# Kernel optimization log

Measured on AMD Instinct MI355X. Metric: run time of the kernel, lower is better.

## Reference

```python
import jax, jax.numpy as jnp
import numpy as np

N_NODES = 100000
N_REL = 7
E = 1600000
D_IN = 128
D_H = 256
D_OUT = 2
EPS = 1e-5


def setup_inputs() -> dict:
    key = jax.random.key(0)
    ks = jax.random.split(key, 16)
    s = 0.05
    features = jax.random.normal(ks[0], (N_NODES, D_IN), jnp.float32)
    edges = jax.random.randint(ks[1], (N_REL, 2, E), 0, N_NODES)
    return {
        "features": features,
        "edges": edges,
        # layer 1 SAGE weights (per relation): fc_self, fc_neigh, bias
        "Wself1": jax.random.normal(ks[2], (N_REL, D_IN, D_H), jnp.float32) * s,
        "Wneigh1": jax.random.normal(ks[3], (N_REL, D_IN, D_H), jnp.float32) * s,
        "b1": jax.random.normal(ks[4], (N_REL, D_H), jnp.float32) * s,
        # layer 2
        "Wself2": jax.random.normal(ks[5], (N_REL, D_H, D_H), jnp.float32) * s,
        "Wneigh2": jax.random.normal(ks[6], (N_REL, D_H, D_H), jnp.float32) * s,
        "b2": jax.random.normal(ks[7], (N_REL, D_H), jnp.float32) * s,
        # LayerNorm params for 2 layers
        "ln_g": jnp.ones((2, D_H), jnp.float32),
        "ln_b": jnp.zeros((2, D_H), jnp.float32),
        # classifier: Linear -> ReLU -> BatchNorm1d(eval) -> Linear
        "Wc1": jax.random.normal(ks[8], (D_H, D_H // 2), jnp.float32) * s,
        "bc1": jnp.zeros((D_H // 2,), jnp.float32),
        "bn_g": jnp.ones((D_H // 2,), jnp.float32),
        "bn_b": jnp.zeros((D_H // 2,), jnp.float32),
        "Wc2": jax.random.normal(ks[9], (D_H // 2, D_OUT), jnp.float32) * s,
        "bc2": jnp.zeros((D_OUT,), jnp.float32),
    }


def _layer_norm(x, g, b):
    mu = jnp.mean(x, axis=-1, keepdims=True)
    var = jnp.var(x, axis=-1, keepdims=True)
    return (x - mu) * jax.lax.rsqrt(var + EPS) * g + b


def _hetero_sage(x, edges, Wself, Wneigh, b):
    # DGL SAGEConv('mean'): out = x @ W_self + mean_neigh(x) @ W_neigh + bias,
    # then HeteroGraphConv aggregate='mean' over relations.
    n = x.shape[0]
    acc = jnp.zeros((n, Wself.shape[-1]), x.dtype)
    for r in range(edges.shape[0]):  # fixed small relation set
        src, dst = edges[r, 0], edges[r, 1]
        msum = jax.ops.segment_sum(x[src], dst, num_segments=n)
        deg = jax.ops.segment_sum(jnp.ones((src.shape[0],), x.dtype), dst, num_segments=n)
        mean = msum / jnp.maximum(deg, 1.0)[:, None]
        acc = acc + x @ Wself[r] + mean @ Wneigh[r] + b[r]
    return acc / edges.shape[0]


def reference(features, edges, Wself1, Wneigh1, b1, Wself2, Wneigh2, b2,
              ln_g, ln_b, Wc1, bc1, bn_g, bn_b, Wc2, bc2):
    # layer 1: hetero conv -> LayerNorm -> ReLU (dropout = identity in eval)
    h = _hetero_sage(features, edges, Wself1, Wneigh1, b1)
    h = jax.nn.relu(_layer_norm(h, ln_g[0], ln_b[0]))
    # layer 2
    h = _hetero_sage(h, edges, Wself2, Wneigh2, b2)
    h = jax.nn.relu(_layer_norm(h, ln_g[1], ln_b[1]))
    # classifier: Linear -> ReLU -> BatchNorm1d(eval: running_mean=0, running_var=1) -> Linear
    z = jax.nn.relu(h @ Wc1 + bc1)
    z = z * (bn_g * jax.lax.rsqrt(jnp.float32(1.0 + EPS))) + bn_b
    return z @ Wc2 + bc2
```

## Files before the change

### kernel.cpp

```cpp
#include <hip/hip_runtime.h>
#include <hip/hip_bf16.h>
#include <cstdint>


#define NN 100000
#define NREL 7
#define NE 1600000
#define NB 128
#define BCAP 14336
#define BNODES 782

using uint = unsigned int;
using ushort_t = unsigned short;
using bf16x8 = __attribute__((ext_vector_type(8))) __bf16;
using f32x4 = __attribute__((ext_vector_type(4))) float;

__device__ __forceinline__ ushort_t f32_to_bf16(float f) {
    uint u = __float_as_uint(f);
    u += 0x7fffu + ((u >> 16) & 1u);
    return (ushort_t)(u >> 16);
}
__device__ __forceinline__ float bf16lo(uint u) { return __uint_as_float(u << 16); }
__device__ __forceinline__ float bf16hi(uint u) { return __uint_as_float(u & 0xffff0000u); }

__device__ __forceinline__ void gload16(const ushort_t* g, ushort_t* l) {
    __builtin_amdgcn_global_load_lds(
        (const __attribute__((address_space(1))) uint*)g,
        (__attribute__((address_space(3))) uint*)l, 16, 0, 0);
}

__global__ __launch_bounds__(256) void binpass_k(const int* __restrict__ edges,
                                                 int* __restrict__ bcnt,
                                                 int* __restrict__ bsrc,
                                                 int* __restrict__ bdst) {
    __shared__ int cnt[NB];
    __shared__ int lofs[NB];
    __shared__ int gbase[NB];
    __shared__ int wtot[2];
    __shared__ int stotal;
    __shared__ uint2 stage[4096];
    __shared__ unsigned char bb[4096];
    int r = blockIdx.y;
    int t = threadIdx.x;
    if (t < NB) cnt[t] = 0;
    __syncthreads();
    int e0 = blockIdx.x * 4096;
    uint2 mypair[16];
    int myrb[16];
#pragma unroll
    for (int i = 0; i < 16; ++i) {
        int e = e0 + i * 256 + t;
        if (e < NE) {
            int s = edges[(size_t)(2 * r) * NE + e];
            int d = edges[(size_t)(2 * r + 1) * NE + e];
            int b = d / BNODES;
            int rank = atomicAdd(&cnt[b], 1);
            myrb[i] = (rank << 7) | b;
            mypair[i] = make_uint2((uint)s, (uint)d);
        } else {
            myrb[i] = -1;
        }
    }
    __syncthreads();
    {
        int c = (t < NB) ? cnt[t] : 0;
        int lane = t & 63, wv = t >> 6;
        int x = c;
#pragma unroll
        for (int off = 1; off < 64; off <<= 1) {
            int y = __shfl_up(x, off);
            if (lane >= off) x += y;
        }
        if (t < NB && lane == 63) wtot[wv] = x;
        __syncthreads();
        if (t < NB) {
            int excl = x - c + (wv ? wtot[0] : 0);
            lofs[t] = excl;
            gbase[t] = atomicAdd(&bcnt[r * NB + t], c);
            if (t == NB - 1) stotal = excl + c;
        }
    }
    __syncthreads();
#pragma unroll
    for (int i = 0; i < 16; ++i) {
        if (myrb[i] >= 0) {
            int b = myrb[i] & 127;
            int p = lofs[b] + (myrb[i] >> 7);
            stage[p] = mypair[i];
            bb[p] = (unsigned char)b;
        }
    }
    __syncthreads();
    int total = stotal;
    for (int p = t; p < total; p += 256) {
        int b = bb[p];
        uint2 pr = stage[p];
        int gpos = gbase[b] + (p - lofs[b]);
        if (gpos < BCAP) {
            size_t o = ((size_t)r * NB + b) * BCAP + gpos;
            bsrc[o] = (int)pr.x;
            bdst[o] = (int)pr.y;
        }
    }
}

__global__ __launch_bounds__(1024) void deg_bucket_k(const int* __restrict__ bdst,
                                                     const int* __restrict__ bcnt,
                                                     int* __restrict__ deg) {
    __shared__ int hist[BNODES];
    int rb = blockIdx.x;
    int r = rb >> 7, b = rb & 127;
    int node0 = b * BNODES;
    int nnodes = NN - node0 < BNODES ? NN - node0 : BNODES;
    int t = threadIdx.x;
    for (int i = t; i < nnodes; i += 1024) hist[i] = 0;
    __syncthreads();
    int cb = bcnt[rb];
    if (cb > BCAP) cb = BCAP;
    const int* src = bdst + (size_t)rb * BCAP;
    for (int i = t; i < cb; i += 1024) {
        atomicAdd(&hist[src[i] - node0], 1);
    }
    __syncthreads();
    for (int i = t; i < nnodes; i += 1024) deg[r * NN + node0 + i] = hist[i];
}

__global__ void scan1_k(const int* __restrict__ deg, int* __restrict__ rowptr,
                        int* __restrict__ blk, int total) {
    __shared__ int wsum[4];
    int t = threadIdx.x;
    int base = blockIdx.x * 4096 + t * 16;
    int vals[16];
    int s = 0;
#pragma unroll
    for (int i = 0; i < 16; ++i) {
        int g = base + i;
        int v = (g < total) ? deg[g] : 0;
        vals[i] = s;
        s += v;
    }
    int lane = t & 63, w = t >> 6;
    int x = s;
    for (int off = 1; off < 64; off <<= 1) {
        int y = __shfl_up(x, off);
        if (lane >= off) x += y;
    }
    if (lane == 63) wsum[w] = x;
    __syncthreads();
    if (t == 0) {
        int a = 0;
#pragma unroll
        for (int k = 0; k < 4; ++k) { int b = wsum[k]; wsum[k] = a; a += b; }
        blk[blockIdx.x] = a;
    }
    __syncthreads();
    int excl = x - s + wsum[w];
#pragma unroll
    for (int i = 0; i < 16; ++i) {
        int g = base + i;
        if (g < total) rowptr[g] = excl + vals[i];
    }
}

__global__ void scan2_k(int* blk, int nb) {
    if (threadIdx.x == 0 && blockIdx.x == 0) {
        int a = 0;
        for (int i = 0; i < nb; ++i) { int b = blk[i]; blk[i] = a; a += b; }
    }
}

__global__ void scan3_k(int* __restrict__ rowptr, const int* __restrict__ blk, int total) {
    int t = threadIdx.x;
    int add = blk[blockIdx.x];
    int base = blockIdx.x * 4096 + t * 16;
#pragma unroll
    for (int i = 0; i < 16; ++i) {
        int g = base + i;
        if (g < total) rowptr[g] += add;
    }
}

__global__ __launch_bounds__(1024) void bucket_sort_k(const int* __restrict__ bsrc,
                                                      const int* __restrict__ bdst,
                                                      const int* __restrict__ bcnt,
                                                      const int* __restrict__ rowptr,
                                                      int* __restrict__ csr) {
    __shared__ int stage[BCAP];
    __shared__ int lcur[BNODES];
    int rb = blockIdx.x;
    int r = rb >> 7, b = rb & 127;
    int node0 = b * BNODES;
    int nnodes = NN - node0 < BNODES ? NN - node0 : BNODES;
    int t = threadIdx.x;
    int rowbase = rowptr[r * NN + node0];
    int endIdx = r * NN + node0 + nnodes;
    int rowend = (endIdx < NREL * NN) ? rowptr[endIdx] : (NREL * NE);
    int truen = rowend - rowbase;
    int nent = truen < BCAP ? truen : BCAP;
    for (int i = t; i < nent; i += 1024) stage[i] = 0;
    for (int i = t; i < nnodes; i += 1024) lcur[i] = 0;
    __syncthreads();
    int cb = bcnt[rb];
    if (cb > BCAP) cb = BCAP;
    for (int i = t; i < cb; i += 1024) {
        int node = bdst[(size_t)rb * BCAP + i];
        int sv = bsrc[(size_t)rb * BCAP + i];
        int pos = rowptr[r * NN + node] - rowbase + atomicAdd(&lcur[node - node0], 1);
        if (pos < BCAP) stage[pos] = sv;
    }
    __syncthreads();
    for (int i = t; i < nent; i += 1024) csr[rowbase + i] = stage[i];
    for (int i = nent + t; i < truen; i += 1024) csr[rowbase + i] = 0;
}

__global__ void convert_x_k(const float* __restrict__ x, ushort_t* __restrict__ xb) {
    int idx = blockIdx.x * 256 + threadIdx.x;
    int n = idx >> 5;
    int c = idx & 31;
    float4 v = *(const float4*)(x + (size_t)n * 128 + c * 4);
    ushort4 o;
    o.x = f32_to_bf16(v.x); o.y = f32_to_bf16(v.y);
    o.z = f32_to_bf16(v.z); o.w = f32_to_bf16(v.w);
    *(ushort4*)(xb + (size_t)n * 128 + c * 4) = o;
}

__global__ void prep_B1cat_k(const float* __restrict__ Wself, const float* __restrict__ Wneigh,
                             const float* __restrict__ b, ushort_t* __restrict__ Bcat,
                             float* __restrict__ bs) {
    int idx = blockIdx.x * 256 + threadIdx.x;
    if (idx < 262144) {
        int n = idx >> 10;
        int k = idx & 1023;
        float v;
        if (k < 128) {
            v = 0.f;
#pragma unroll
            for (int r = 0; r < 7; ++r) v += Wself[((size_t)r * 128 + k) * 256 + n];
        } else {
            int rel = (k >> 7) - 1;
            int k2 = k & 127;
            v = Wneigh[((size_t)rel * 128 + k2) * 256 + n];
        }
        Bcat[(size_t)n * 1024 + k] = f32_to_bf16(v);
    } else if (idx < 262400) {
        int i = idx - 262144;
        float s = 0.f;
#pragma unroll
        for (int r = 0; r < 7; ++r) s += b[r * 256 + i];
        bs[i] = s * (1.f / 7.f);
    }
}

__global__ void prep_B2cat_k(const float* __restrict__ Wself, const float* __restrict__ Wneigh,
                             const float* __restrict__ b, ushort_t* __restrict__ Bcat,
                             float* __restrict__ bs) {
    int idx = blockIdx.x * 256 + threadIdx.x;
    if (idx < 524288) {
        int n = idx >> 11;
        int k = idx & 2047;
        float v;
        if (k < 256) {
            v = 0.f;
#pragma unroll
            for (int r = 0; r < 7; ++r) v += Wself[((size_t)r * 256 + k) * 256 + n];
        } else {
            int rel = (k >> 8) - 1;
            int k2 = k & 255;
            v = Wneigh[((size_t)rel * 256 + k2) * 256 + n];
        }
        Bcat[(size_t)n * 2048 + k] = f32_to_bf16(v);
    } else if (idx < 524544) {
        int i = idx - 524288;
        float s = 0.f;
#pragma unroll
        for (int r = 0; r < 7; ++r) s += b[r * 256 + i];
        bs[i] = s * (1.f / 7.f);
    }
}

__global__ void prep_cls_k(const float* __restrict__ Wc1, const float* __restrict__ bn_g,
                           const float* __restrict__ bn_b, const float* __restrict__ Wc2,
                           const float* __restrict__ bc2, ushort_t* __restrict__ Wc1T,
                           float* __restrict__ W2p, float* __restrict__ cp) {
    int idx = blockIdx.x * 256 + threadIdx.x;
    if (idx < 128 * 256) {
        int n = idx >> 8;
        int k = idx & 255;
        Wc1T[(size_t)n * 256 + k] = f32_to_bf16(Wc1[(size_t)k * 128 + n]);
    } else if (idx < 128 * 256 + 256) {
        int e = idx - 128 * 256;
        int d = e >> 1, j = e & 1;
        W2p[e] = bn_g[d] * rsqrtf(1.f + 1e-5f) * Wc2[d * 2 + j];
    } else if (idx < 128 * 256 + 256 + 2) {
        int j = idx - (128 * 256 + 256);
        float s = bc2[j];
        for (int d = 0; d < 128; ++d) s += bn_b[d] * Wc2[d * 2 + j];
        cp[j] = s;
    }
}

template <int V>
__global__ __launch_bounds__(256) void gather_mean_k(
    const ushort_t* __restrict__ T, const int* __restrict__ csr,
    const int* __restrict__ rowptr, const int* __restrict__ deg,
    ushort_t* __restrict__ Mout, int r, int n0) {
    int n = n0 + blockIdx.x * 4 + (threadIdx.x >> 6);
    if (n >= NN) return;
    int lane = threadIdx.x & 63;
    int pair = r * NN + n;
    int start = rowptr[pair];
    int cnt = deg[pair];
    float aLo[2][2] = {{0.f, 0.f}, {0.f, 0.f}};
    float aHi[2][2] = {{0.f, 0.f}, {0.f, 0.f}};
    int j = 0;
    if (V == 1) {
        const uint* Tu = (const uint*)T;
        for (; j + 8 <= cnt; j += 8) {
            int s[8];
#pragma unroll
            for (int q = 0; q < 8; ++q) s[q] = csr[start + j + q];
            uint u[8];
#pragma unroll
            for (int q = 0; q < 8; ++q) u[q] = Tu[(size_t)s[q] * 64 + lane];
#pragma unroll
            for (int q = 0; q < 8; ++q) {
                aLo[0][q & 1] += bf16lo(u[q]);
                aHi[0][q & 1] += bf16hi(u[q]);
            }
        }
        for (; j < cnt; ++j) {
            uint u = Tu[(size_t)csr[start + j] * 64 + lane];
            aLo[0][0] += bf16lo(u);
            aHi[0][0] += bf16hi(u);
        }
        float inv = 1.f / (float)(cnt > 1 ? cnt : 1);
        uint lo = f32_to_bf16((aLo[0][0] + aLo[0][1]) * inv);
        uint hi = f32_to_bf16((aHi[0][0] + aHi[0][1]) * inv);
        ((uint*)(Mout + (size_t)(n - n0) * 128))[lane] = lo | (hi << 16);
    } else {
        const uint2* Tu = (const uint2*)T;
        for (; j + 8 <= cnt; j += 8) {
            int s[8];
#pragma unroll
            for (int q = 0; q < 8; ++q) s[q] = csr[start + j + q];
            uint2 u[8];
#pragma unroll
            for (int q = 0; q < 8; ++q) u[q] = Tu[(size_t)s[q] * 64 + lane];
#pragma unroll
            for (int q = 0; q < 8; ++q) {
                aLo[0][q & 1] += bf16lo(u[q].x);
                aHi[0][q & 1] += bf16hi(u[q].x);
                aLo[1][q & 1] += bf16lo(u[q].y);
                aHi[1][q & 1] += bf16hi(u[q].y);
            }
        }
        for (; j < cnt; ++j) {
            uint2 u = Tu[(size_t)csr[start + j] * 64 + lane];
            aLo[0][0] += bf16lo(u.x);
            aHi[0][0] += bf16hi(u.x);
            aLo[1][0] += bf16lo(u.y);
            aHi[1][0] += bf16hi(u.y);
        }
        float inv = 1.f / (float)(cnt > 1 ? cnt : 1);
        uint lox = f32_to_bf16((aLo[0][0] + aLo[0][1]) * inv);
        uint hix = f32_to_bf16((aHi[0][0] + aHi[0][1]) * inv);
        uint loy = f32_to_bf16((aLo[1][0] + aLo[1][1]) * inv);
        uint hiy = f32_to_bf16((aHi[1][0] + aHi[1][1]) * inv);
        ((uint2*)(Mout + (size_t)(n - n0) * 256))[lane] =
            make_uint2(lox | (hix << 16), loy | (hiy << 16));
    }
}

__global__ __launch_bounds__(256) void gemm_multi(
    const ushort_t* __restrict__ A0, const ushort_t* __restrict__ AM,
    int D, int lgD, int aoff, int Mseg, const ushort_t* __restrict__ BT,
    void* __restrict__ Cv, int M, int N, int K, float alpha,
    const float* __restrict__ bias, int mode) {
    __shared__ __align__(16) ushort_t lA[2 * 4096];
    __shared__ __align__(16) ushort_t lB[2 * 4096];
    int t = threadIdx.x;
    int gr0 = blockIdx.x * 128;
    int gc0 = blockIdx.y * 128;
    int w = t >> 6, lane = t & 63;
    int wr = w >> 1, wc = w & 1;
    int lm = lane & 15, quad = lane >> 4;
    int srow = lane >> 2;
    int schunk = (lane & 3) * 8;
    const ushort_t* A0s = A0 + (size_t)aoff * D;
    size_t segstride = (size_t)Mseg * D;
    f32x4 acc[4][4];
#pragma unroll
    for (int i = 0; i < 4; ++i)
#pragma unroll
        for (int j = 0; j < 4; ++j) acc[i][j] = (f32x4){0.f, 0.f, 0.f, 0.f};

    for (int kk = 0; kk < K; kk += 64) {
        int seg = kk >> lgD;
        int kloc = kk & (D - 1);
        const ushort_t* Asrc = (seg == 0) ? A0s : (AM + (size_t)(seg - 1) * segstride);
        __syncthreads();
#pragma unroll
        for (int s = 0; s < 2; ++s) {
#pragma unroll
            for (int j = 0; j < 2; ++j) {
                int rb = (j * 4 + w) * 16;
                int row = rb + srow;
                int gr = gr0 + row;
                if (gr < M)
                    gload16(Asrc + (size_t)gr * D + kloc + s * 32 + schunk,
                            lA + s * 4096 + rb * 32);
                gload16(BT + (size_t)(gc0 + row) * K + kk + s * 32 + schunk,
                        lB + s * 4096 + rb * 32);
            }
        }
        __syncthreads();
#pragma unroll
        for (int s = 0; s < 2; ++s) {
            bf16x8 af[4], bfr[4];
#pragma unroll
            for (int f = 0; f < 4; ++f) {
                af[f] = *(const bf16x8*)(lA + s * 4096 + (wr * 64 + f * 16 + lm) * 32 + quad * 8);
                bfr[f] = *(const bf16x8*)(lB + s * 4096 + (wc * 64 + f * 16 + lm) * 32 + quad * 8);
            }
#pragma unroll
            for (int fr = 0; fr < 4; ++fr)
#pragma unroll
                for (int fc = 0; fc < 4; ++fc)
                    acc[fr][fc] = __builtin_amdgcn_mfma_f32_16x16x32_bf16(
                        af[fr], bfr[fc], acc[fr][fc], 0, 0, 0);
        }
    }
    float* Cf = (float*)Cv;
    ushort_t* Cb = (ushort_t*)Cv;
#pragma unroll
    for (int fr = 0; fr < 4; ++fr) {
#pragma unroll
        for (int fc = 0; fc < 4; ++fc) {
#pragma unroll
            for (int i = 0; i < 4; ++i) {
                int row = wr * 64 + fr * 16 + quad * 4 + i;
                int col = wc * 64 + fc * 16 + lm;
                int gr = gr0 + row;
                int gc = gc0 + col;
                if (gr < M) {
                    size_t o = (size_t)gr * N + gc;
                    float v = acc[fr][fc][i] * alpha;
                    v += bias ? bias[gc] : 0.f;
                    if (mode == 4) {
                        Cf[o] = fmaxf(v, 0.f);
                    } else {
                        Cb[o] = f32_to_bf16(v);
                    }
                }
            }
        }
    }
}

__global__ __launch_bounds__(256) void ln_relu_b_k(
    const ushort_t* __restrict__ h, const float* __restrict__ g,
    const float* __restrict__ b, ushort_t* __restrict__ out) {
    int n = blockIdx.x * 4 + (threadIdx.x >> 6);
    if (n >= NN) return;
    int lane = threadIdx.x & 63;
    uint2 u = ((const uint2*)(h + (size_t)n * 256))[lane];
    float v0 = bf16lo(u.x), v1 = bf16hi(u.x), v2 = bf16lo(u.y), v3 = bf16hi(u.y);
    float s = v0 + v1 + v2 + v3;
    float q = v0 * v0 + v1 * v1 + v2 * v2 + v3 * v3;
#pragma unroll
    for (int m = 1; m < 64; m <<= 1) {
        s += __shfl_xor(s, m);
        q += __shfl_xor(q, m);
    }
    float mean = s * (1.f / 256.f);
    float var = q * (1.f / 256.f) - mean * mean;
    float rs = rsqrtf(var + 1e-5f);
    float4 gv = *(const float4*)(g + lane * 4);
    float4 bv = *(const float4*)(b + lane * 4);
    float y0 = fmaxf((v0 - mean) * rs * gv.x + bv.x, 0.f);
    float y1 = fmaxf((v1 - mean) * rs * gv.y + bv.y, 0.f);
    float y2 = fmaxf((v2 - mean) * rs * gv.z + bv.z, 0.f);
    float y3 = fmaxf((v3 - mean) * rs * gv.w + bv.w, 0.f);
    uint2 o;
    o.x = (uint)f32_to_bf16(y0) | ((uint)f32_to_bf16(y1) << 16);
    o.y = (uint)f32_to_bf16(y2) | ((uint)f32_to_bf16(y3) << 16);
    *(uint2*)(out + (size_t)n * 256 + lane * 4) = o;
}

__global__ __launch_bounds__(256) void final_k(const float* __restrict__ z1,
                                               const float* __restrict__ W2p,
                                               const float* __restrict__ cp,
                                               float* __restrict__ out) {
    int n = blockIdx.x * 4 + (threadIdx.x >> 6);
    if (n >= NN) return;
    int lane = threadIdx.x & 63;
    const float* zr = z1 + (size_t)n * 128;
    float z0 = zr[lane], z1v = zr[lane + 64];
    float a0 = z0 * W2p[lane * 2 + 0] + z1v * W2p[(lane + 64) * 2 + 0];
    float a1 = z0 * W2p[lane * 2 + 1] + z1v * W2p[(lane + 64) * 2 + 1];
#pragma unroll
    for (int m = 1; m < 64; m <<= 1) {
        a0 += __shfl_xor(a0, m);
        a1 += __shfl_xor(a1, m);
    }
    if (lane == 0) {
        out[(size_t)n * 2 + 0] = a0 + cp[0];
        out[(size_t)n * 2 + 1] = a1 + cp[1];
    }
}

constexpr size_t O_DEG   = 0;
constexpr size_t O_ROW   = 2800128;
constexpr size_t O_BLK   = 5600256;
constexpr size_t O_CSR   = 5601280;
constexpr size_t O_B1C   = 50401280;
constexpr size_t O_B2C   = 50925568;
constexpr size_t O_WC1T  = 51974144;
constexpr size_t O_W2P   = 52039680;
constexpr size_t O_CP    = 52040704;
constexpr size_t O_B1S   = 52040960;
constexpr size_t O_B2S   = 52041984;
constexpr size_t O_XB    = 52043008;
constexpr size_t O_MEAN1 = 77643008;
constexpr size_t O_HACC1 = 167243008;
constexpr size_t O_BCNT  = 52043008;
constexpr size_t O_BSRC  = 52047104;
constexpr size_t O_BDST  = 103427328;
constexpr size_t O_H1B   = O_XB;
constexpr size_t O_MEAN2 = 103243008;
constexpr size_t O_HACC2 = 192843008;
constexpr size_t O_H2B   = O_XB;
constexpr size_t O_Z1    = O_MEAN2;
constexpr size_t WS_REQUIRED = 244043008;

extern "C" void kernel_launch(void* const* d_in, const int* in_sizes, int n_in,
                              void* d_out, int out_size, void* d_ws, size_t ws_size,
                              hipStream_t stream) {
    (void)in_sizes; (void)n_in;
    const float* features = (const float*)d_in[0];
    const int* edges = (const int*)d_in[1];
    const float* Wself1 = (const float*)d_in[2];
    const float* Wneigh1 = (const float*)d_in[3];
    const float* b1 = (const float*)d_in[4];
    const float* Wself2 = (const float*)d_in[5];
    const float* Wneigh2 = (const float*)d_in[6];
    const float* b2 = (const float*)d_in[7];
    const float* ln_g = (const float*)d_in[8];
    const float* ln_b = (const float*)d_in[9];
    const float* Wc1 = (const float*)d_in[10];
    const float* bc1 = (const float*)d_in[11];
    const float* bn_g = (const float*)d_in[12];
    const float* bn_b = (const float*)d_in[13];
    const float* Wc2 = (const float*)d_in[14];
    const float* bc2 = (const float*)d_in[15];
    float* out = (float*)d_out;
    char* ws = (char*)d_ws;

    if (ws_size < WS_REQUIRED) {
        hipMemsetAsync(d_out, 0, (size_t)out_size * 4, stream);
        return;
    }

    int* deg = (int*)(ws + O_DEG);
    int* rowptr = (int*)(ws + O_ROW);
    int* blk = (int*)(ws + O_BLK);
    int* csr = (int*)(ws + O_CSR);
    ushort_t* B1cat = (ushort_t*)(ws + O_B1C);
    ushort_t* B2cat = (ushort_t*)(ws + O_B2C);
    ushort_t* Wc1T = (ushort_t*)(ws + O_WC1T);
    float* W2p = (float*)(ws + O_W2P);
    float* cp = (float*)(ws + O_CP);
    float* b1s = (float*)(ws + O_B1S);
    float* b2s = (float*)(ws + O_B2S);
    ushort_t* xb = (ushort_t*)(ws + O_XB);
    ushort_t* mean1 = (ushort_t*)(ws + O_MEAN1);
    ushort_t* hacc1 = (ushort_t*)(ws + O_HACC1);
    ushort_t* h1b = (ushort_t*)(ws + O_H1B);
    ushort_t* mean2 = (ushort_t*)(ws + O_MEAN2);
    ushort_t* hacc2 = (ushort_t*)(ws + O_HACC2);
    ushort_t* h2b = (ushort_t*)(ws + O_H2B);
    float* z1 = (float*)(ws + O_Z1);
    int* bcnt = (int*)(ws + O_BCNT);
    int* bsrc = (int*)(ws + O_BSRC);
    int* bdst = (int*)(ws + O_BDST);

    hipMemsetAsync(ws + O_BCNT, 0, 4096, stream);

    binpass_k<<<dim3(391, 7, 1), 256, 0, stream>>>(edges, bcnt, bsrc, bdst);
    deg_bucket_k<<<896, 1024, 0, stream>>>(bdst, bcnt, deg);
    scan1_k<<<171, 256, 0, stream>>>(deg, rowptr, blk, NREL * NN);
    scan2_k<<<1, 64, 0, stream>>>(blk, 171);
    scan3_k<<<171, 256, 0, stream>>>(rowptr, blk, NREL * NN);
    bucket_sort_k<<<896, 1024, 0, stream>>>(bsrc, bdst, bcnt, rowptr, csr);

    convert_x_k<<<12500, 256, 0, stream>>>(features, xb);
    prep_B1cat_k<<<1025, 256, 0, stream>>>(Wself1, Wneigh1, b1, B1cat, b1s);
    prep_B2cat_k<<<2050, 256, 0, stream>>>(Wself2, Wneigh2, b2, B2cat, b2s);
    prep_cls_k<<<130, 256, 0, stream>>>(Wc1, bn_g, bn_b, Wc2, bc2, Wc1T, W2p, cp);

    for (int h = 0; h < 2; ++h) {
        int n0 = h * 50000;
        for (int r = 0; r < 7; ++r)
            gather_mean_k<1><<<12500, 256, 0, stream>>>(
                xb, csr, rowptr, deg, mean1 + (size_t)r * 50000 * 128, r, n0);
        gemm_multi<<<dim3(391, 2, 1), 256, 0, stream>>>(
            xb, mean1, 128, 7, n0, 50000, B1cat,
            hacc1 + (size_t)n0 * 256, 50000, 256, 1024, 1.f / 7.f, b1s, 2);
    }
    ln_relu_b_k<<<25000, 256, 0, stream>>>(hacc1, ln_g, ln_b, h1b);

    for (int q = 0; q < 4; ++q) {
        int n0 = q * 25000;
        for (int r = 0; r < 7; ++r)
            gather_mean_k<2><<<6250, 256, 0, stream>>>(
                h1b, csr, rowptr, deg, mean2 + (size_t)r * 25000 * 256, r, n0);
        gemm_multi<<<dim3(196, 2, 1), 256, 0, stream>>>(
            h1b, mean2, 256, 8, n0, 25000, B2cat,
            hacc2 + (size_t)n0 * 256, 25000, 256, 2048, 1.f / 7.f, b2s, 2);
    }
    ln_relu_b_k<<<25000, 256, 0, stream>>>(hacc2, ln_g + 256, ln_b + 256, h2b);

    gemm_multi<<<dim3(782, 1, 1), 256, 0, stream>>>(
        h2b, nullptr, 256, 8, 0, 0, Wc1T, z1, NN, 128, 256, 1.f, bc1, 4);
    final_k<<<25000, 256, 0, stream>>>(z1, W2p, cp, out);
}
```

Measured before the change: 2.232 ms.

## Pack bucketed edges into one word, batch relation gathers, add larger-workspace path

Binned edges are stored as a single 32-bit word (source shifted by 10 bits, OR'd with the local destination) instead of two int arrays. This halves the bucket traffic in binpass, deg_bucket and bucket_sort. The gather_mean kernel now handles all 7 relations in one launch via blockIdx.y and uses a predicated, clamped 8-wide loop in place of the scalar tail. When the workspace is large enough, a new path processes layer 1 in one chunk and layer 2 in two chunks, cutting launch count. The packing assumes source ids fit in 22 bits, and the full path only runs if the harness provides at least 333 MB of workspace.

```diff
diff --git a/kernel.cpp b/kernel.cpp
--- a/kernel.cpp
+++ b/kernel.cpp
@@ -31,21 +31,20 @@
 
 __global__ __launch_bounds__(256) void binpass_k(const int* __restrict__ edges,
                                                  int* __restrict__ bcnt,
-                                                 int* __restrict__ bsrc,
-                                                 int* __restrict__ bdst) {
+                                                 uint* __restrict__ bpack) {
     __shared__ int cnt[NB];
     __shared__ int lofs[NB];
     __shared__ int gbase[NB];
     __shared__ int wtot[2];
     __shared__ int stotal;
-    __shared__ uint2 stage[4096];
+    __shared__ uint stage[4096];
     __shared__ unsigned char bb[4096];
     int r = blockIdx.y;
     int t = threadIdx.x;
     if (t < NB) cnt[t] = 0;
     __syncthreads();
     int e0 = blockIdx.x * 4096;
-    uint2 mypair[16];
+    uint mypack[16];
     int myrb[16];
 #pragma unroll
     for (int i = 0; i < 16; ++i) {
@@ -54,9 +53,10 @@
             int s = edges[(size_t)(2 * r) * NE + e];
             int d = edges[(size_t)(2 * r + 1) * NE + e];
             int b = d / BNODES;
+            int dl = d - b * BNODES;
             int rank = atomicAdd(&cnt[b], 1);
             myrb[i] = (rank << 7) | b;
-            mypair[i] = make_uint2((uint)s, (uint)d);
+            mypack[i] = ((uint)s << 10) | (uint)dl;
         } else {
             myrb[i] = -1;
         }
@@ -86,7 +86,7 @@
         if (myrb[i] >= 0) {
             int b = myrb[i] & 127;
             int p = lofs[b] + (myrb[i] >> 7);
-            stage[p] = mypair[i];
+            stage[p] = mypack[i];
             bb[p] = (unsigned char)b;
         }
     }
@@ -94,17 +94,15 @@
     int total = stotal;
     for (int p = t; p < total; p += 256) {
         int b = bb[p];
-        uint2 pr = stage[p];
+        uint pr = stage[p];
         int gpos = gbase[b] + (p - lofs[b]);
         if (gpos < BCAP) {
-            size_t o = ((size_t)r * NB + b) * BCAP + gpos;
-            bsrc[o] = (int)pr.x;
-            bdst[o] = (int)pr.y;
-        }
-    }
-}
-
-__global__ __launch_bounds__(1024) void deg_bucket_k(const int* __restrict__ bdst,
+            bpack[((size_t)r * NB + b) * BCAP + gpos] = pr;
+        }
+    }
+}
+
+__global__ __launch_bounds__(1024) void deg_bucket_k(const uint* __restrict__ bpack,
                                                      const int* __restrict__ bcnt,
                                                      int* __restrict__ deg) {
     __shared__ int hist[BNODES];
@@ -117,9 +115,9 @@
     __syncthreads();
     int cb = bcnt[rb];
     if (cb > BCAP) cb = BCAP;
-    const int* src = bdst + (size_t)rb * BCAP;
+    const uint* src = bpack + (size_t)rb * BCAP;
     for (int i = t; i < cb; i += 1024) {
-        atomicAdd(&hist[src[i] - node0], 1);
+        atomicAdd(&hist[src[i] & 1023u], 1);
     }
     __syncthreads();
     for (int i = t; i < nnodes; i += 1024) deg[r * NN + node0 + i] = hist[i];
@@ -180,8 +178,7 @@
     }
 }
 
-__global__ __launch_bounds__(1024) void bucket_sort_k(const int* __restrict__ bsrc,
-                                                      const int* __restrict__ bdst,
+__global__ __launch_bounds__(1024) void bucket_sort_k(const uint* __restrict__ bpack,
                                                       const int* __restrict__ bcnt,
                                                       const int* __restrict__ rowptr,
                                                       int* __restrict__ csr) {
@@ -203,9 +200,10 @@
     int cb = bcnt[rb];
     if (cb > BCAP) cb = BCAP;
     for (int i = t; i < cb; i += 1024) {
-        int node = bdst[(size_t)rb * BCAP + i];
-        int sv = bsrc[(size_t)rb * BCAP + i];
-        int pos = rowptr[r * NN + node] - rowbase + atomicAdd(&lcur[node - node0], 1);
+        uint v = bpack[(size_t)rb * BCAP + i];
+        int nl = (int)(v & 1023u);
+        int sv = (int)(v >> 10);
+        int pos = rowptr[r * NN + node0 + nl] - rowbase + atomicAdd(&lcur[nl], 1);
         if (pos < BCAP) stage[pos] = sv;
     }
     __syncthreads();
@@ -303,65 +301,67 @@
 __global__ __launch_bounds__(256) void gather_mean_k(
     const ushort_t* __restrict__ T, const int* __restrict__ csr,
     const int* __restrict__ rowptr, const int* __restrict__ deg,
-    ushort_t* __restrict__ Mout, int r, int n0) {
+    ushort_t* __restrict__ M0, int n0, int sliceM) {
+    int r = blockIdx.y;
     int n = n0 + blockIdx.x * 4 + (threadIdx.x >> 6);
     if (n >= NN) return;
     int lane = threadIdx.x & 63;
+    ushort_t* Mout = M0 + (size_t)r * sliceM * (V * 128);
     int pair = r * NN + n;
-    int start = rowptr[pair];
-    int cnt = deg[pair];
-    float aLo[2][2] = {{0.f, 0.f}, {0.f, 0.f}};
-    float aHi[2][2] = {{0.f, 0.f}, {0.f, 0.f}};
-    int j = 0;
+    int start = __builtin_amdgcn_readfirstlane(rowptr[pair]);
+    int cnt = __builtin_amdgcn_readfirstlane(deg[pair]);
+    int cm1 = (cnt > 0) ? (cnt - 1) : 0;
+    if (cnt <= 0) start = 0;
+    const int* cp = csr + start;
+    float inv = 1.f / (float)(cnt > 1 ? cnt : 1);
     if (V == 1) {
         const uint* Tu = (const uint*)T;
-        for (; j + 8 <= cnt; j += 8) {
+        float aLo[2] = {0.f, 0.f}, aHi[2] = {0.f, 0.f};
+        for (int j = 0; j < cnt; j += 8) {
             int s[8];
-#pragma unroll
-            for (int q = 0; q < 8; ++q) s[q] = csr[start + j + q];
             uint u[8];
 #pragma unroll
+            for (int q = 0; q < 8; ++q) {
+                int e = j + q;
+                s[q] = cp[e < cm1 ? e : cm1];
+            }
+#pragma unroll
             for (int q = 0; q < 8; ++q) u[q] = Tu[(size_t)s[q] * 64 + lane];
 #pragma unroll
             for (int q = 0; q < 8; ++q) {
-                aLo[0][q & 1] += bf16lo(u[q]);
-                aHi[0][q & 1] += bf16hi(u[q]);
+                uint m = (j + q < cnt) ? u[q] : 0u;
+                aLo[q & 1] += bf16lo(m);
+                aHi[q & 1] += bf16hi(m);
             }
         }
-        for (; j < cnt; ++j) {
-            uint u = Tu[(size_t)csr[start + j] * 64 + lane];
-            aLo[0][0] += bf16lo(u);
-            aHi[0][0] += bf16hi(u);
-        }
-        float inv = 1.f / (float)(cnt > 1 ? cnt : 1);
-        uint lo = f32_to_bf16((aLo[0][0] + aLo[0][1]) * inv);
-        uint hi = f32_to_bf16((aHi[0][0] + aHi[0][1]) * inv);
+        uint lo = f32_to_bf16((aLo[0] + aLo[1]) * inv);
+        uint hi = f32_to_bf16((aHi[0] + aHi[1]) * inv);
         ((uint*)(Mout + (size_t)(n - n0) * 128))[lane] = lo | (hi << 16);
     } else {
         const uint2* Tu = (const uint2*)T;
-        for (; j + 8 <= cnt; j += 8) {
+        float aLo[2][2] = {{0.f, 0.f}, {0.f, 0.f}};
+        float aHi[2][2] = {{0.f, 0.f}, {0.f, 0.f}};
+        for (int j = 0; j < cnt; j += 8) {
             int s[8];
-#pragma unroll
-            for (int q = 0; q < 8; ++q) s[q] = csr[start + j + q];
             uint2 u[8];
 #pragma unroll
+            for (int q = 0; q < 8; ++q) {
+                int e = j + q;
+                s[q] = cp[e < cm1 ? e : cm1];
+            }
+#pragma unroll
             for (int q = 0; q < 8; ++q) u[q] = Tu[(size_t)s[q] * 64 + lane];
 #pragma unroll
             for (int q = 0; q < 8; ++q) {
-                aLo[0][q & 1] += bf16lo(u[q].x);
-                aHi[0][q & 1] += bf16hi(u[q].x);
-                aLo[1][q & 1] += bf16lo(u[q].y);
-                aHi[1][q & 1] += bf16hi(u[q].y);
+                bool ok = (j + q < cnt);
+                uint mx = ok ? u[q].x : 0u;
+                uint my = ok ? u[q].y : 0u;
+                aLo[0][q & 1] += bf16lo(mx);
+                aHi[0][q & 1] += bf16hi(mx);
+                aLo[1][q & 1] += bf16lo(my);
+                aHi[1][q & 1] += bf16hi(my);
             }
         }
-        for (; j < cnt; ++j) {
-            uint2 u = Tu[(size_t)csr[start + j] * 64 + lane];
-            aLo[0][0] += bf16lo(u.x);
-            aHi[0][0] += bf16hi(u.x);
-            aLo[1][0] += bf16lo(u.y);
-            aHi[1][0] += bf16hi(u.y);
-        }
-        float inv = 1.f / (float)(cnt > 1 ? cnt : 1);
         uint lox = f32_to_bf16((aLo[0][0] + aLo[0][1]) * inv);
         uint hix = f32_to_bf16((aHi[0][0] + aHi[0][1]) * inv);
         uint loy = f32_to_bf16((aLo[1][0] + aLo[1][1]) * inv);
@@ -521,17 +521,24 @@
 constexpr size_t O_B1S   = 52040960;
 constexpr size_t O_B2S   = 52041984;
 constexpr size_t O_XB    = 52043008;
-constexpr size_t O_MEAN1 = 77643008;
-constexpr size_t O_HACC1 = 167243008;
 constexpr size_t O_BCNT  = 52043008;
-constexpr size_t O_BSRC  = 52047104;
-constexpr size_t O_BDST  = 103427328;
-constexpr size_t O_H1B   = O_XB;
-constexpr size_t O_MEAN2 = 103243008;
-constexpr size_t O_HACC2 = 192843008;
-constexpr size_t O_H2B   = O_XB;
-constexpr size_t O_Z1    = O_MEAN2;
-constexpr size_t WS_REQUIRED = 244043008;
+constexpr size_t O_BPK   = 52047104;
+constexpr size_t OF_MEAN1 = 77643008;
+constexpr size_t OF_HACC1 = 256843008;
+constexpr size_t OF_H1B   = 52043008;
+constexpr size_t OF_MEAN2 = 103243008;
+constexpr size_t OF_HACC2 = 282443008;
+constexpr size_t OF_H2B   = 52043008;
+constexpr size_t OF_Z1    = 103243008;
+constexpr size_t WS_FULL  = 333643008;
+constexpr size_t OQ_MEAN1 = 77643008;
+constexpr size_t OQ_HACC1 = 167243008;
+constexpr size_t OQ_H1B   = 52043008;
+constexpr size_t OQ_MEAN2 = 103243008;
+constexpr size_t OQ_HACC2 = 192843008;
+constexpr size_t OQ_H2B   = 52043008;
+constexpr size_t OQ_Z1    = 103243008;
+constexpr size_t WS_QUART = 244043008;
 
 extern "C" void kernel_launch(void* const* d_in, const int* in_sizes, int n_in,
                               void* d_out, int out_size, void* d_ws, size_t ws_size,
@@ -556,10 +563,11 @@
     float* out = (float*)d_out;
     char* ws = (char*)d_ws;
 
-    if (ws_size < WS_REQUIRED) {
+    if (ws_size < WS_QUART) {
         hipMemsetAsync(d_out, 0, (size_t)out_size * 4, stream);
         return;
     }
+    bool full = (ws_size >= WS_FULL);
 
     int* deg = (int*)(ws + O_DEG);
     int* rowptr = (int*)(ws + O_ROW);
@@ -573,52 +581,69 @@
     float* b1s = (float*)(ws + O_B1S);
     float* b2s = (float*)(ws + O_B2S);
     ushort_t* xb = (ushort_t*)(ws + O_XB);
-    ushort_t* mean1 = (ushort_t*)(ws + O_MEAN1);
-    ushort_t* hacc1 = (ushort_t*)(ws + O_HACC1);
-    ushort_t* h1b = (ushort_t*)(ws + O_H1B);
-    ushort_t* mean2 = (ushort_t*)(ws + O_MEAN2);
-    ushort_t* hacc2 = (ushort_t*)(ws + O_HACC2);
-    ushort_t* h2b = (ushort_t*)(ws + O_H2B);
-    float* z1 = (float*)(ws + O_Z1);
     int* bcnt = (int*)(ws + O_BCNT);
-    int* bsrc = (int*)(ws + O_BSRC);
-    int* bdst = (int*)(ws + O_BDST);
-
-    hipMemsetAsync(ws + O_BCNT, 0, 4096, stream);
-
-    binpass_k<<<dim3(391, 7, 1), 256, 0, stream>>>(edges, bcnt, bsrc, bdst);
-    deg_bucket_k<<<896, 1024, 0, stream>>>(bdst, bcnt, deg);
+    uint* bpack = (uint*)(ws + O_BPK);
+
+    ushort_t* mean1 = (ushort_t*)(ws + (full ? OF_MEAN1 : OQ_MEAN1));
+    ushort_t* hacc1 = (ushort_t*)(ws + (full ? OF_HACC1 : OQ_HACC1));
+    ushort_t* h1b   = (ushort_t*)(ws + (full ? OF_H1B : OQ_H1B));
+    ushort_t* mean2 = (ushort_t*)(ws + (full ? OF_MEAN2 : OQ_MEAN2));
+    ushort_t* hacc2 = (ushort_t*)(ws + (full ? OF_HACC2 : OQ_HACC2));
+    ushort_t* h2b   = (ushort_t*)(ws + (full ? OF_H2B : OQ_H2B));
+    float* z1       = (float*)(ws + (full ? OF_Z1 : OQ_Z1));
+
+    hipMemsetAsync(bcnt, 0, 4096, stream);
+
+    binpass_k<<<dim3(391, 7, 1), 256, 0, stream>>>(edges, bcnt, bpack);
+    deg_bucket_k<<<896, 1024, 0, stream>>>(bpack, bcnt, deg);
     scan1_k<<<171, 256, 0, stream>>>(deg, rowptr, blk, NREL * NN);
     scan2_k<<<1, 64, 0, stream>>>(blk, 171);
     scan3_k<<<171, 256, 0, stream>>>(rowptr, blk, NREL * NN);
-    bucket_sort_k<<<896, 1024, 0, stream>>>(bsrc, bdst, bcnt, rowptr, csr);
+    bucket_sort_k<<<896, 1024, 0, stream>>>(bpack, bcnt, rowptr, csr);
 
     convert_x_k<<<12500, 256, 0, stream>>>(features, xb);
     prep_B1cat_k<<<1025, 256, 0, stream>>>(Wself1, Wneigh1, b1, B1cat, b1s);
     prep_B2cat_k<<<2050, 256, 0, stream>>>(Wself2, Wneigh2, b2, B2cat, b2s);
     prep_cls_k<<<130, 256, 0, stream>>>(Wc1, bn_g, bn_b, Wc2, bc2, Wc1T, W2p, cp);
 
-    for (int h = 0; h < 2; ++h) {
-        int n0 = h * 50000;
-        for (int r = 0; r < 7; ++r)
-            gather_mean_k<1><<<12500, 256, 0, stream>>>(
-                xb, csr, rowptr, deg, mean1 + (size_t)r * 50000 * 128, r, n0);
-        gemm_multi<<<dim3(391, 2, 1), 256, 0, stream>>>(
-            xb, mean1, 128, 7, n0, 50000, B1cat,
-            hacc1 + (size_t)n0 * 256, 50000, 256, 1024, 1.f / 7.f, b1s, 2);
-    }
-    ln_relu_b_k<<<25000, 256, 0, stream>>>(hacc1, ln_g, ln_b, h1b);
-
-    for (int q = 0; q < 4; ++q) {
-        int n0 = q * 25000;
-        for (int r = 0; r < 7; ++r)
-            gather_mean_k<2><<<6250, 256, 0, stream>>>(
-                h1b, csr, rowptr, deg, mean2 + (size_t)r * 25000 * 256, r, n0);
-        gemm_multi<<<dim3(196, 2, 1), 256, 0, stream>>>(
-            h1b, mean2, 256, 8, n0, 25000, B2cat,
-            hacc2 + (size_t)n0 * 256, 25000, 256, 2048, 1.f / 7.f, b2s, 2);
-    }
-    ln_relu_b_k<<<25000, 256, 0, stream>>>(hacc2, ln_g + 256, ln_b + 256, h2b);
+    if (full) {
+        gather_mean_k<1><<<dim3(25000, 7, 1), 256, 0, stream>>>(
+            xb, csr, rowptr, deg, mean1, 0, 100000);
+        gemm_multi<<<dim3(782, 2, 1), 256, 0, stream>>>(
+            xb, mean1, 128, 7, 0, 100000, B1cat,
+            hacc1, 100000, 256, 1024, 1.f / 7.f, b1s, 2);
+        ln_relu_b_k<<<25000, 256, 0, stream>>>(hacc1, ln_g, ln_b, h1b);
+
+        for (int h = 0; h < 2; ++h) {
+            int n0 = h * 50000;
+            gather_mean_k<2><<<dim3(12500, 7, 1), 256, 0, stream>>>(
+                h1b, csr, rowptr, deg, mean2, n0, 50000);
+            gemm_multi<<<dim3(391, 2, 1), 256, 0, stream>>>(
+                h1b, mean2, 256, 8, n0, 50000, B2cat,
+                hacc2 + (size_t)n0 * 256, 50000, 256, 2048, 1.f / 7.f, b2s, 2);
+        }
+        ln_relu_b_k<<<25000, 256, 0, stream>>>(hacc2, ln_g + 256, ln_b + 256, h2b);
+    } else {
+        for (int h = 0; h < 2; ++h) {
+            int n0 = h * 50000;
+            gather_mean_k<1><<<dim3(12500, 7, 1), 256, 0, stream>>>(
+                xb, csr, rowptr, deg, mean1, n0, 50000);
+            gemm_multi<<<dim3(391, 2, 1), 256, 0, stream>>>(
+                xb, mean1, 128, 7, n0, 50000, B1cat,
+                hacc1 + (size_t)n0 * 256, 50000, 256, 1024, 1.f / 7.f, b1s, 2);
+        }
+        ln_relu_b_k<<<25000, 256, 0, stream>>>(hacc1, ln_g, ln_b, h1b);
+
+        for (int q = 0; q < 4; ++q) {
+            int n0 = q * 25000;
+            gather_mean_k<2><<<dim3(6250, 7, 1), 256, 0, stream>>>(
+                h1b, csr, rowptr, deg, mean2, n0, 25000);
+            gemm_multi<<<dim3(196, 2, 1), 256, 0, stream>>>(
+                h1b, mean2, 256, 8, n0, 25000, B2cat,
+                hacc2 + (size_t)n0 * 256, 25000, 256, 2048, 1.f / 7.f, b2s, 2);
+        }
+        ln_relu_b_k<<<25000, 256, 0, stream>>>(hacc2, ln_g + 256, ln_b + 256, h2b);
+    }
 
     gemm_multi<<<dim3(782, 1, 1), 256, 0, stream>>>(
         h2b, nullptr, 256, 8, 0, 0, Wc1T, z1, NN, 128, 256, 1.f, bc1, 4);
```

Result: faster. 1.876 ms (-16.0%).
